# Kernel optimization log

Hardware: AMD Instinct MI355X
Metric: run time of the kernel (lower is better)

The kernel has to match this reference:

```python
import jax, jax.numpy as jnp
import numpy as np

BN_EPS = 1e-5

def _conv1x1(x, w, b):
    # x: [B,C,H,W], w: [O,C], b: [O] -> [B,O,H,W]
    return jnp.einsum('bchw,oc->bohw', x, w) + b[None, :, None, None]

def setup_inputs() -> dict:
    key = jax.random.key(0)
    ks = jax.random.split(key, 9)
    B, C, H, W = 8, 256, 64, 64
    I = C // 2
    s_in = 1.0 / np.sqrt(C)
    s_out = 1.0 / np.sqrt(I)
    return {
        'x':       jax.random.normal(ks[0], (B, C, H, W), dtype=jnp.float32),
        'g_w':     jax.random.uniform(ks[1], (I, C), jnp.float32, -s_in, s_in),
        'g_b':     jax.random.uniform(ks[2], (I,),  jnp.float32, -s_in, s_in),
        'theta_w': jax.random.uniform(ks[3], (I, C), jnp.float32, -s_in, s_in),
        'theta_b': jax.random.uniform(ks[4], (I,),  jnp.float32, -s_in, s_in),
        'phi_w':   jax.random.uniform(ks[5], (I, C), jnp.float32, -s_in, s_in),
        'phi_b':   jax.random.uniform(ks[6], (I,),  jnp.float32, -s_in, s_in),
        'w_w':     jax.random.uniform(ks[7], (C, I), jnp.float32, -s_out, s_out),
        'w_b':     jax.random.uniform(ks[8], (C,),  jnp.float32, -s_out, s_out),
        'gamma':   jnp.ones((C,), dtype=jnp.float32),   # BN weight init constant 1
        'beta':    jnp.zeros((C,), dtype=jnp.float32),  # BN bias init constant 0
    }

def reference(x, g_w, g_b, theta_w, theta_b, phi_w, phi_b, w_w, w_b, gamma, beta):
    B, C, H, W = x.shape
    I = g_w.shape[0]
    N = H * W
    g_x     = _conv1x1(x, g_w, g_b).reshape(B, I, N)          # [B,I,N]
    theta_x = _conv1x1(x, theta_w, theta_b).reshape(B, I, N)  # [B,I,N]
    phi_x   = _conv1x1(x, phi_w, phi_b).reshape(B, I, N)      # [B,I,N]
    # f = theta^T @ phi : [B,N,N]
    f = jnp.einsum('bin,bim->bnm', theta_x, phi_x)
    a = jax.nn.softmax(f, axis=-1)
    # y = a @ g^T : [B,N,I] -> [B,I,H,W]
    y = jnp.einsum('bnm,bim->bin', a, g_x).reshape(B, I, H, W)
    wy = _conv1x1(y, w_w, w_b)                                # [B,C,H,W]
    # BatchNorm2d (training mode: batch statistics over B,H,W per channel)
    mean = jnp.mean(wy, axis=(0, 2, 3), keepdims=True)
    var = jnp.var(wy, axis=(0, 2, 3), keepdims=True)
    wy_bn = (wy - mean) * jax.lax.rsqrt(var + BN_EPS)
    wy_bn = wy_bn * gamma[None, :, None, None] + beta[None, :, None, None]
    return wy_bn + x
```

## Files before the change

kernel.cpp:

```cpp
#include <hip/hip_runtime.h>

#define B_ 8
#define C_ 256
#define I_ 128
#define N_ 4096
#define BN_ (B_ * N_)
#define LOG2E 1.4426950408889634f

typedef __attribute__((ext_vector_type(8))) short bf16x8;
typedef __attribute__((ext_vector_type(4))) float f32x4;

static __device__ __forceinline__ short f2bf(float f) {
    unsigned u = __float_as_uint(f);
    unsigned r = u + 0x7fffu + ((u >> 16) & 1u);
    return (short)(r >> 16);
}
static __device__ __forceinline__ float bf2f(short s) {
    return __uint_as_float(((unsigned)(unsigned short)s) << 16);
}

__global__ void k_prep(const float* g_w, const float* theta_w, const float* phi_w,
                       const float* g_b, const float* theta_b, const float* phi_b,
                       const float* w_w, short* wcat, short* wwb, float* bcat) {
    int i = blockIdx.x * 256 + threadIdx.x;
    if (i < 384 * 256) {
        int j = i >> 8, c = i & 255;
        float v = (j < 128) ? theta_w[j * 256 + c] * LOG2E
                : (j < 256) ? phi_w[(j - 128) * 256 + c]
                            : g_w[(j - 256) * 256 + c];
        wcat[i] = f2bf(v);
    } else if (i < 384 * 256 + 256 * 128) {
        int k = i - 384 * 256;
        wwb[k] = f2bf(w_w[k]);
    } else if (i < 384 * 256 + 256 * 128 + 384) {
        int j = i - (384 * 256 + 256 * 128);
        bcat[j] = (j < 128) ? theta_b[j] * LOG2E
                : (j < 256) ? phi_b[j - 128] : g_b[j - 256];
    }
}

__global__ __launch_bounds__(256) void k_proj(const float* __restrict__ x,
                                              const short* __restrict__ wcat,
                                              const float* __restrict__ bcat,
                                              short* __restrict__ tp,
                                              short* __restrict__ gmat) {
    int b = blockIdx.y;
    int n0 = blockIdx.x * 64;
    int tid = threadIdx.x;
    int wave = tid >> 6, lane = tid & 63, s = lane & 15, q = lane >> 4;
    __shared__ short xs[64][264];

#pragma unroll
    for (int it = 0; it < 16; ++it) {
        int cr = (tid >> 4) + it * 16;
        int nc = tid & 15;
        const float4 v = *(const float4*)&x[((size_t)b * C_ + cr) * N_ + n0 + nc * 4];
        xs[nc * 4 + 0][cr] = f2bf(v.x);
        xs[nc * 4 + 1][cr] = f2bf(v.y);
        xs[nc * 4 + 2][cr] = f2bf(v.z);
        xs[nc * 4 + 3][cr] = f2bf(v.w);
    }
    __syncthreads();

    f32x4 acc[4][6];
#pragma unroll
    for (int rt = 0; rt < 4; ++rt)
#pragma unroll
        for (int jt = 0; jt < 6; ++jt) acc[rt][jt] = (f32x4){0.f, 0.f, 0.f, 0.f};

#pragma unroll
    for (int kb = 0; kb < 8; ++kb) {
        bf16x8 af[4], bfv[6];
#pragma unroll
        for (int rt = 0; rt < 4; ++rt)
            af[rt] = *(const bf16x8*)&xs[rt * 16 + s][kb * 32 + q * 8];
#pragma unroll
        for (int jt = 0; jt < 6; ++jt)
            bfv[jt] = *(const bf16x8*)&wcat[(wave * 96 + jt * 16 + s) * 256 + kb * 32 + q * 8];
#pragma unroll
        for (int rt = 0; rt < 4; ++rt)
#pragma unroll
            for (int jt = 0; jt < 6; ++jt)
                acc[rt][jt] = __builtin_amdgcn_mfma_f32_16x16x32_bf16(af[rt], bfv[jt], acc[rt][jt], 0, 0, 0);
    }

#pragma unroll
    for (int rt = 0; rt < 4; ++rt)
#pragma unroll
        for (int jt = 0; jt < 6; ++jt) {
            int j = wave * 96 + jt * 16 + s;
            float bias = bcat[j];
#pragma unroll
            for (int r = 0; r < 4; ++r) {
                int n = n0 + rt * 16 + 4 * q + r;
                float v = acc[rt][jt][r] + bias;
                if (j < 256)
                    tp[((size_t)b * N_ + n) * 256 + j] = f2bf(v);
                else
                    gmat[((size_t)b * I_ + (j - 256)) * N_ + n] = f2bf(v);
            }
        }
}

__global__ __launch_bounds__(256) void k_attn(const short* __restrict__ tp,
                                              const short* __restrict__ gmat,
                                              float* __restrict__ Op,
                                              float* __restrict__ lbuf) {
    int id = blockIdx.x;
    int b = id & 7;
    int qt = (id >> 3) & 31;
    int half = id >> 8;
    int n0 = qt * 128;
    int tid = threadIdx.x;
    int wave = tid >> 6, lane = tid & 63, s = lane & 15, q = lane >> 4;

    __shared__ short Kt[64][136];
    __shared__ short Vt[128][72];
    __shared__ short Pl[4][32][68];

    bf16x8 qf[2][4];
#pragma unroll
    for (int fr = 0; fr < 2; ++fr) {
        const short* qb = tp + ((size_t)b * N_ + n0 + wave * 32 + fr * 16 + s) * 256;
#pragma unroll
        for (int kb = 0; kb < 4; ++kb) qf[fr][kb] = *(const bf16x8*)(qb + kb * 32 + q * 8);
    }

    f32x4 ot[2][8];
#pragma unroll
    for (int fr = 0; fr < 2; ++fr)
#pragma unroll
        for (int t = 0; t < 8; ++t) ot[fr][t] = (f32x4){0.f, 0.f, 0.f, 0.f};
    float lsum[2][4] = {{0.f, 0.f, 0.f, 0.f}, {0.f, 0.f, 0.f, 0.f}};

    const int mStart = half * 2048, mEnd = mStart + 2048;
    int krow = (tid >> 4), kch = tid & 15;
    int vrow = (tid >> 3), vch = tid & 7;

    bf16x8 pk[4], pv[4];
#pragma unroll
    for (int it = 0; it < 4; ++it) {
        pk[it] = *(const bf16x8*)&tp[((size_t)b * N_ + mStart + krow + it * 16) * 256 + 128 + kch * 8];
        pv[it] = *(const bf16x8*)&gmat[((size_t)b * I_ + vrow + it * 32) * N_ + mStart + vch * 8];
    }

    for (int m0 = mStart; m0 < mEnd; m0 += 64) {
        __syncthreads();
#pragma unroll
        for (int it = 0; it < 4; ++it) {
            *(bf16x8*)&Kt[krow + it * 16][kch * 8] = pk[it];
            *(bf16x8*)&Vt[vrow + it * 32][vch * 8] = pv[it];
        }
        __syncthreads();
        if (m0 + 64 < mEnd) {
#pragma unroll
            for (int it = 0; it < 4; ++it) {
                pk[it] = *(const bf16x8*)&tp[((size_t)b * N_ + m0 + 64 + krow + it * 16) * 256 + 128 + kch * 8];
                pv[it] = *(const bf16x8*)&gmat[((size_t)b * I_ + vrow + it * 32) * N_ + m0 + 64 + vch * 8];
            }
        }

        f32x4 sa[2][4];
#pragma unroll
        for (int fr = 0; fr < 2; ++fr)
#pragma unroll
            for (int tc = 0; tc < 4; ++tc) sa[fr][tc] = (f32x4){0.f, 0.f, 0.f, 0.f};
#pragma unroll
        for (int tc = 0; tc < 4; ++tc) {
            bf16x8 bfv[4];
#pragma unroll
            for (int kb = 0; kb < 4; ++kb)
                bfv[kb] = *(const bf16x8*)&Kt[tc * 16 + s][kb * 32 + q * 8];
#pragma unroll
            for (int fr = 0; fr < 2; ++fr)
#pragma unroll
                for (int kb = 0; kb < 4; ++kb)
                    sa[fr][tc] = __builtin_amdgcn_mfma_f32_16x16x32_bf16(qf[fr][kb], bfv[kb], sa[fr][tc], 0, 0, 0);
        }

#pragma unroll
        for (int fr = 0; fr < 2; ++fr) {
#pragma unroll
            for (int tc = 0; tc < 4; ++tc)
#pragma unroll
                for (int r = 0; r < 4; ++r) sa[fr][tc][r] = exp2f(sa[fr][tc][r]);
#pragma unroll
            for (int r = 0; r < 4; ++r)
                lsum[fr][r] += (sa[fr][0][r] + sa[fr][1][r]) + (sa[fr][2][r] + sa[fr][3][r]);
#pragma unroll
            for (int tc = 0; tc < 4; ++tc)
#pragma unroll
                for (int r = 0; r < 4; ++r)
                    Pl[wave][fr * 16 + 4 * q + r][tc * 16 + s] = f2bf(sa[fr][tc][r]);
        }

#pragma unroll
        for (int kb2 = 0; kb2 < 2; ++kb2) {
            bf16x8 pa0 = *(const bf16x8*)&Pl[wave][s][kb2 * 32 + q * 8];
            bf16x8 pa1 = *(const bf16x8*)&Pl[wave][16 + s][kb2 * 32 + q * 8];
#pragma unroll
            for (int t = 0; t < 8; ++t) {
                bf16x8 vb = *(const bf16x8*)&Vt[t * 16 + s][kb2 * 32 + q * 8];
                ot[0][t] = __builtin_amdgcn_mfma_f32_16x16x32_bf16(pa0, vb, ot[0][t], 0, 0, 0);
                ot[1][t] = __builtin_amdgcn_mfma_f32_16x16x32_bf16(pa1, vb, ot[1][t], 0, 0, 0);
            }
        }
    }

#pragma unroll
    for (int fr = 0; fr < 2; ++fr)
#pragma unroll
        for (int r = 0; r < 4; ++r) {
#pragma unroll
            for (int off = 1; off < 16; off <<= 1)
                lsum[fr][r] += __shfl_xor(lsum[fr][r], off);
        }
    if (s == 0) {
#pragma unroll
        for (int fr = 0; fr < 2; ++fr)
#pragma unroll
            for (int r = 0; r < 4; ++r) {
                size_t row = (size_t)half * BN_ + (size_t)b * N_ + n0 + wave * 32 + fr * 16 + 4 * q + r;
                lbuf[row] = lsum[fr][r];
            }
    }

#pragma unroll
    for (int fr = 0; fr < 2; ++fr) {
        size_t rbase = (size_t)half * BN_ + (size_t)b * N_ + n0 + wave * 32 + fr * 16 + 4 * q;
#pragma unroll
        for (int t = 0; t < 8; ++t)
#pragma unroll
            for (int r = 0; r < 4; ++r)
                Op[(rbase + r) * I_ + t * 16 + s] = ot[fr][t][r];
    }
}

__global__ __launch_bounds__(256) void k_wy(const float* __restrict__ Op,
                                            const float* __restrict__ lbuf,
                                            const short* __restrict__ wwb,
                                            const float* __restrict__ w_b,
                                            short* __restrict__ wyh) {
    int b = blockIdx.y;
    int n0 = blockIdx.x * 64;
    int tid = threadIdx.x;
    int wave = tid >> 6, lane = tid & 63, s = lane & 15, q = lane >> 4;

    float linv[4];
#pragma unroll
    for (int nt = 0; nt < 4; ++nt) {
        size_t rn = (size_t)b * N_ + n0 + nt * 16 + s;
        linv[nt] = 1.0f / (lbuf[rn] + lbuf[(size_t)BN_ + rn]);
    }

    f32x4 acc[4][4];
#pragma unroll
    for (int ct = 0; ct < 4; ++ct)
#pragma unroll
        for (int nt = 0; nt < 4; ++nt) acc[ct][nt] = (f32x4){0.f, 0.f, 0.f, 0.f};
#pragma unroll
    for (int kb = 0; kb < 4; ++kb) {
        bf16x8 af[4], bfv[4];
#pragma unroll
        for (int ct = 0; ct < 4; ++ct)
            af[ct] = *(const bf16x8*)&wwb[(wave * 64 + ct * 16 + s) * 128 + kb * 32 + q * 8];
#pragma unroll
        for (int nt = 0; nt < 4; ++nt) {
            size_t rn = (size_t)b * N_ + n0 + nt * 16 + s;
            const float* p1 = Op + rn * I_ + kb * 32 + q * 8;
            const float* p2 = p1 + (size_t)BN_ * I_;
            float4 a0 = *(const float4*)p1;
            float4 a1 = *(const float4*)(p1 + 4);
            float4 b0 = *(const float4*)p2;
            float4 b1 = *(const float4*)(p2 + 4);
            short v[8];
            v[0] = f2bf((a0.x + b0.x) * linv[nt]);
            v[1] = f2bf((a0.y + b0.y) * linv[nt]);
            v[2] = f2bf((a0.z + b0.z) * linv[nt]);
            v[3] = f2bf((a0.w + b0.w) * linv[nt]);
            v[4] = f2bf((a1.x + b1.x) * linv[nt]);
            v[5] = f2bf((a1.y + b1.y) * linv[nt]);
            v[6] = f2bf((a1.z + b1.z) * linv[nt]);
            v[7] = f2bf((a1.w + b1.w) * linv[nt]);
            bfv[nt] = *(const bf16x8*)v;
        }
#pragma unroll
        for (int ct = 0; ct < 4; ++ct)
#pragma unroll
            for (int nt = 0; nt < 4; ++nt)
                acc[ct][nt] = __builtin_amdgcn_mfma_f32_16x16x32_bf16(af[ct], bfv[nt], acc[ct][nt], 0, 0, 0);
    }
#pragma unroll
    for (int ct = 0; ct < 4; ++ct)
#pragma unroll
        for (int nt = 0; nt < 4; ++nt)
#pragma unroll
            for (int r = 0; r < 4; ++r) {
                int c = wave * 64 + ct * 16 + 4 * q + r;
                int n = n0 + nt * 16 + s;
                wyh[((size_t)b * C_ + c) * N_ + n] = f2bf(acc[ct][nt][r] + w_b[c]);
            }
}

__global__ __launch_bounds__(256) void k_stats(const short* __restrict__ wyh,
                                               const float* __restrict__ gamma,
                                               const float* __restrict__ beta,
                                               float* __restrict__ scale,
                                               float* __restrict__ shift) {
    int c = blockIdx.x;
    int tid = threadIdx.x;
    float s1 = 0.f, s2 = 0.f;
    for (int b = 0; b < B_; ++b) {
        const short* p = wyh + ((size_t)b * C_ + c) * N_;
        for (int idx = tid * 8; idx < N_; idx += 2048) {
            bf16x8 v = *(const bf16x8*)&p[idx];
#pragma unroll
            for (int j = 0; j < 8; ++j) {
                float f = bf2f(v[j]);
                s1 += f;
                s2 += f * f;
            }
        }
    }
#pragma unroll
    for (int off = 1; off < 64; off <<= 1) {
        s1 += __shfl_xor(s1, off);
        s2 += __shfl_xor(s2, off);
    }
    __shared__ float r1[4], r2[4];
    if ((tid & 63) == 0) { r1[tid >> 6] = s1; r2[tid >> 6] = s2; }
    __syncthreads();
    if (tid == 0) {
        float t1 = r1[0] + r1[1] + r1[2] + r1[3];
        float t2 = r2[0] + r2[1] + r2[2] + r2[3];
        const float inv = 1.0f / 32768.0f;
        float mean = t1 * inv;
        float var = t2 * inv - mean * mean;
        float sc = gamma[c] * rsqrtf(var + 1e-5f);
        scale[c] = sc;
        shift[c] = beta[c] - mean * sc;
    }
}

__global__ __launch_bounds__(256) void k_out(const short* __restrict__ wyh,
                                             const float* __restrict__ x,
                                             const float* __restrict__ scale,
                                             const float* __restrict__ shift,
                                             float* __restrict__ out) {
    int gid = blockIdx.x * 256 + threadIdx.x;
    size_t base = (size_t)gid * 8;
    int c = (int)((base >> 12) & 255);
    float sc = scale[c], sh = shift[c];
    bf16x8 w = *(const bf16x8*)&wyh[base];
    float4 x0 = *(const float4*)&x[base];
    float4 x1 = *(const float4*)&x[base + 4];
    float4 o0, o1;
    o0.x = bf2f(w[0]) * sc + sh + x0.x;
    o0.y = bf2f(w[1]) * sc + sh + x0.y;
    o0.z = bf2f(w[2]) * sc + sh + x0.z;
    o0.w = bf2f(w[3]) * sc + sh + x0.w;
    o1.x = bf2f(w[4]) * sc + sh + x1.x;
    o1.y = bf2f(w[5]) * sc + sh + x1.y;
    o1.z = bf2f(w[6]) * sc + sh + x1.z;
    o1.w = bf2f(w[7]) * sc + sh + x1.w;
    *(float4*)&out[base] = o0;
    *(float4*)&out[base + 4] = o1;
}

extern "C" void kernel_launch(void* const* d_in, const int* in_sizes, int n_in,
                              void* d_out, int out_size, void* d_ws, size_t ws_size,
                              hipStream_t stream) {
    const float* x       = (const float*)d_in[0];
    const float* g_w     = (const float*)d_in[1];
    const float* g_b     = (const float*)d_in[2];
    const float* theta_w = (const float*)d_in[3];
    const float* theta_b = (const float*)d_in[4];
    const float* phi_w   = (const float*)d_in[5];
    const float* phi_b   = (const float*)d_in[6];
    const float* w_w     = (const float*)d_in[7];
    const float* w_b     = (const float*)d_in[8];
    const float* gamma   = (const float*)d_in[9];
    const float* beta    = (const float*)d_in[10];

    char* ws = (char*)d_ws;
    size_t off = 0;
    auto alloc = [&](size_t bytes) {
        void* p = ws + off;
        off += (bytes + 255) & ~(size_t)255;
        return p;
    };
    short*  wcat  = (short*)alloc((size_t)384 * 256 * 2);
    short*  wwb   = (short*)alloc((size_t)256 * 128 * 2);
    float*  bcat  = (float*)alloc((size_t)384 * 4);
    float*  scale = (float*)alloc(256 * 4);
    float*  shift = (float*)alloc(256 * 4);
    short*  tp    = (short*)alloc((size_t)BN_ * 256 * 2);
    short*  gmat  = (short*)alloc((size_t)B_ * I_ * N_ * 2);
    short*  wyh   = (short*)alloc((size_t)BN_ * C_ * 2);
    float*  lbuf  = (float*)alloc((size_t)2 * BN_ * 4);
    float*  Op    = (float*)d_out;

    k_prep<<<514, 256, 0, stream>>>(g_w, theta_w, phi_w, g_b, theta_b, phi_b, w_w,
                                    wcat, wwb, bcat);
    k_proj<<<dim3(64, 8), 256, 0, stream>>>(x, wcat, bcat, tp, gmat);
    k_attn<<<512, 256, 0, stream>>>(tp, gmat, Op, lbuf);
    k_wy<<<dim3(64, 8), 256, 0, stream>>>(Op, lbuf, wwb, w_b, wyh);
    k_stats<<<256, 256, 0, stream>>>(wyh, gamma, beta, scale, shift);
    k_out<<<4096, 256, 0, stream>>>(wyh, x, scale, shift, (float*)d_out);
}
```

Measured before the change: 264.6 us.

## Swizzle attention LDS tiles, transpose QK MFMA, and pack P bf16 stores

Replaces padded shared-memory arrays for K, V and P with unpadded XOR-swizzled layouts, so LDS reads and writes avoid bank conflicts without padding. The QK^T MFMA operands are swapped so each lane holds scores for one query row. Row sums can then be reduced in-lane plus two shuffles, and P can be written as packed 8-byte stores using v_cvt_pk_bf16_f32. This is meant to cut LDS bank conflicts, scalar store count and shuffle work, at the cost of more complex address arithmetic and inline asm.

New measurement: 253.0 us. 4.4% less time.

```diff
diff --git a/kernel.cpp b/kernel.cpp
--- a/kernel.cpp
+++ b/kernel.cpp
@@ -9,6 +9,7 @@
 
 typedef __attribute__((ext_vector_type(8))) short bf16x8;
 typedef __attribute__((ext_vector_type(4))) float f32x4;
+typedef __attribute__((ext_vector_type(2))) int i32x2;
 
 static __device__ __forceinline__ short f2bf(float f) {
     unsigned u = __float_as_uint(f);
@@ -17,6 +18,11 @@
 }
 static __device__ __forceinline__ float bf2f(short s) {
     return __uint_as_float(((unsigned)(unsigned short)s) << 16);
+}
+static __device__ __forceinline__ unsigned cvt_pk_bf16(float lo, float hi) {
+    unsigned r;
+    asm("v_cvt_pk_bf16_f32 %0, %1, %2" : "=v"(r) : "v"(lo), "v"(hi));
+    return r;
 }
 
 __global__ void k_prep(const float* g_w, const float* theta_w, const float* phi_w,
@@ -114,9 +120,34 @@
     int tid = threadIdx.x;
     int wave = tid >> 6, lane = tid & 63, s = lane & 15, q = lane >> 4;
 
-    __shared__ short Kt[64][136];
-    __shared__ short Vt[128][72];
-    __shared__ short Pl[4][32][68];
+    __shared__ __align__(16) short Kt[64 * 128];
+    __shared__ __align__(16) short Vt[128 * 64];
+    __shared__ __align__(16) short Pl[4 * 32 * 64];
+
+    char* KtB = (char*)Kt;
+    char* VtB = (char*)Vt;
+    char* PlB = (char*)Pl;
+
+    const int swz = (s & 7) << 4;
+    int kA[4];
+#pragma unroll
+    for (int kb = 0; kb < 4; ++kb) kA[kb] = s * 256 + ((kb * 64 + q * 16) ^ swz);
+    int vA[2];
+    int pR[2];
+#pragma unroll
+    for (int kb2 = 0; kb2 < 2; ++kb2) {
+        int col = (kb2 * 64 + q * 16) ^ swz;
+        vA[kb2] = s * 128 + col;
+        pR[kb2] = wave * 4096 + s * 128 + col;
+    }
+    int pW[4];
+#pragma unroll
+    for (int tc = 0; tc < 4; ++tc)
+        pW[tc] = wave * 4096 + s * 128 + ((tc * 32 + q * 8) ^ swz);
+    int krow = tid >> 4, kch = tid & 15;
+    int vrow = tid >> 3, vch = tid & 7;
+    int kW = krow * 256 + ((kch * 16) ^ ((krow & 7) << 4));
+    int vW = vrow * 128 + ((vch * 16) ^ ((vrow & 7) << 4));
 
     bf16x8 qf[2][4];
 #pragma unroll
@@ -131,11 +162,9 @@
     for (int fr = 0; fr < 2; ++fr)
 #pragma unroll
         for (int t = 0; t < 8; ++t) ot[fr][t] = (f32x4){0.f, 0.f, 0.f, 0.f};
-    float lsum[2][4] = {{0.f, 0.f, 0.f, 0.f}, {0.f, 0.f, 0.f, 0.f}};
+    float lsum[2] = {0.f, 0.f};
 
     const int mStart = half * 2048, mEnd = mStart + 2048;
-    int krow = (tid >> 4), kch = tid & 15;
-    int vrow = (tid >> 3), vch = tid & 7;
 
     bf16x8 pk[4], pv[4];
 #pragma unroll
@@ -148,8 +177,8 @@
         __syncthreads();
 #pragma unroll
         for (int it = 0; it < 4; ++it) {
-            *(bf16x8*)&Kt[krow + it * 16][kch * 8] = pk[it];
-            *(bf16x8*)&Vt[vrow + it * 32][vch * 8] = pv[it];
+            *(bf16x8*)(KtB + kW + it * 4096) = pk[it];
+            *(bf16x8*)(VtB + vW + it * 4096) = pv[it];
         }
         __syncthreads();
         if (m0 + 64 < mEnd) {
@@ -170,12 +199,12 @@
             bf16x8 bfv[4];
 #pragma unroll
             for (int kb = 0; kb < 4; ++kb)
-                bfv[kb] = *(const bf16x8*)&Kt[tc * 16 + s][kb * 32 + q * 8];
+                bfv[kb] = *(const bf16x8*)(KtB + kA[kb] + tc * 4096);
 #pragma unroll
             for (int fr = 0; fr < 2; ++fr)
 #pragma unroll
                 for (int kb = 0; kb < 4; ++kb)
-                    sa[fr][tc] = __builtin_amdgcn_mfma_f32_16x16x32_bf16(qf[fr][kb], bfv[kb], sa[fr][tc], 0, 0, 0);
+                    sa[fr][tc] = __builtin_amdgcn_mfma_f32_16x16x32_bf16(bfv[kb], qf[fr][kb], sa[fr][tc], 0, 0, 0);
         }
 
 #pragma unroll
@@ -184,23 +213,27 @@
             for (int tc = 0; tc < 4; ++tc)
 #pragma unroll
                 for (int r = 0; r < 4; ++r) sa[fr][tc][r] = exp2f(sa[fr][tc][r]);
-#pragma unroll
-            for (int r = 0; r < 4; ++r)
-                lsum[fr][r] += (sa[fr][0][r] + sa[fr][1][r]) + (sa[fr][2][r] + sa[fr][3][r]);
-#pragma unroll
-            for (int tc = 0; tc < 4; ++tc)
-#pragma unroll
-                for (int r = 0; r < 4; ++r)
-                    Pl[wave][fr * 16 + 4 * q + r][tc * 16 + s] = f2bf(sa[fr][tc][r]);
+            float t0 = (sa[fr][0][0] + sa[fr][0][1]) + (sa[fr][0][2] + sa[fr][0][3]);
+            float t1 = (sa[fr][1][0] + sa[fr][1][1]) + (sa[fr][1][2] + sa[fr][1][3]);
+            float t2 = (sa[fr][2][0] + sa[fr][2][1]) + (sa[fr][2][2] + sa[fr][2][3]);
+            float t3 = (sa[fr][3][0] + sa[fr][3][1]) + (sa[fr][3][2] + sa[fr][3][3]);
+            lsum[fr] += (t0 + t1) + (t2 + t3);
+#pragma unroll
+            for (int tc = 0; tc < 4; ++tc) {
+                i32x2 w;
+                w.x = (int)cvt_pk_bf16(sa[fr][tc][0], sa[fr][tc][1]);
+                w.y = (int)cvt_pk_bf16(sa[fr][tc][2], sa[fr][tc][3]);
+                *(i32x2*)(PlB + pW[tc] + fr * 2048) = w;
+            }
         }
 
 #pragma unroll
         for (int kb2 = 0; kb2 < 2; ++kb2) {
-            bf16x8 pa0 = *(const bf16x8*)&Pl[wave][s][kb2 * 32 + q * 8];
-            bf16x8 pa1 = *(const bf16x8*)&Pl[wave][16 + s][kb2 * 32 + q * 8];
+            bf16x8 pa0 = *(const bf16x8*)(PlB + pR[kb2]);
+            bf16x8 pa1 = *(const bf16x8*)(PlB + pR[kb2] + 2048);
 #pragma unroll
             for (int t = 0; t < 8; ++t) {
-                bf16x8 vb = *(const bf16x8*)&Vt[t * 16 + s][kb2 * 32 + q * 8];
+                bf16x8 vb = *(const bf16x8*)(VtB + vA[kb2] + t * 2048);
                 ot[0][t] = __builtin_amdgcn_mfma_f32_16x16x32_bf16(pa0, vb, ot[0][t], 0, 0, 0);
                 ot[1][t] = __builtin_amdgcn_mfma_f32_16x16x32_bf16(pa1, vb, ot[1][t], 0, 0, 0);
             }
@@ -208,21 +241,16 @@
     }
 
 #pragma unroll
-    for (int fr = 0; fr < 2; ++fr)
-#pragma unroll
-        for (int r = 0; r < 4; ++r) {
-#pragma unroll
-            for (int off = 1; off < 16; off <<= 1)
-                lsum[fr][r] += __shfl_xor(lsum[fr][r], off);
-        }
-    if (s == 0) {
-#pragma unroll
-        for (int fr = 0; fr < 2; ++fr)
-#pragma unroll
-            for (int r = 0; r < 4; ++r) {
-                size_t row = (size_t)half * BN_ + (size_t)b * N_ + n0 + wave * 32 + fr * 16 + 4 * q + r;
-                lbuf[row] = lsum[fr][r];
-            }
+    for (int fr = 0; fr < 2; ++fr) {
+        lsum[fr] += __shfl_xor(lsum[fr], 16);
+        lsum[fr] += __shfl_xor(lsum[fr], 32);
+    }
+    if (q == 0) {
+#pragma unroll
+        for (int fr = 0; fr < 2; ++fr) {
+            size_t row = (size_t)half * BN_ + (size_t)b * N_ + n0 + wave * 32 + fr * 16 + s;
+            lbuf[row] = lsum[fr];
+        }
     }
 
 #pragma unroll
```
